# Kernel optimization log

Measured on AMD Instinct MI355X. Metric: run time of the kernel, lower is better.

The kernel has to match this reference:

```python
import jax, jax.numpy as jnp
import numpy as np

B, S, HID, H, DB = 4, 2048, 512, 8, 8
DH = HID // H  # head dim = 64


def setup_inputs() -> dict:
    key = jax.random.key(0)
    ks = jax.random.split(key, 14)
    s = 0.02
    return {
        "q": jax.random.normal(ks[0], (B, S, HID), jnp.float32),
        "k": jax.random.normal(ks[1], (B, S, HID), jnp.float32),
        "v": jax.random.normal(ks[2], (B, S, HID), jnp.float32),
        "attn_bias": jax.random.normal(ks[3], (B, S, S, DB), jnp.float32),
        "Wq": jax.random.normal(ks[4], (HID, HID), jnp.float32) * s,
        "bq": jnp.zeros((HID,), jnp.float32),
        "Wk": jax.random.normal(ks[5], (HID, HID), jnp.float32) * s,
        "bk": jnp.zeros((HID,), jnp.float32),
        "Wv": jax.random.normal(ks[6], (HID, HID), jnp.float32) * s,
        "bv": jnp.zeros((HID,), jnp.float32),
        "Wb": jax.random.normal(ks[7], (H, DB), jnp.float32) * s,
        "bb": jnp.zeros((H,), jnp.float32),
        "Wo": jax.random.normal(ks[8], (HID, HID), jnp.float32) * s,
        "bo": jnp.zeros((HID,), jnp.float32),
    }


def reference(q, k, v, attn_bias, Wq, bq, Wk, bk, Wv, bv, Wb, bb, Wo, bo):
    scale = DH ** (-0.5)
    # projections: torch Linear is x @ W.T + b
    qh = (q @ Wq.T + bq).reshape(B, S, H, DH).transpose(0, 2, 1, 3)  # [B,H,S,D]
    kh = (k @ Wk.T + bk).reshape(B, S, H, DH).transpose(0, 2, 1, 3)
    vh = (v @ Wv.T + bv).reshape(B, S, H, DH).transpose(0, 2, 1, 3)
    scores = jnp.einsum("bhqd,bhkd->bhqk", qh * scale, kh)  # [B,H,S,S]
    bias = (attn_bias @ Wb.T + bb).transpose(0, 3, 1, 2)  # [B,H,S,S]
    attn = jax.nn.softmax(scores + bias, axis=-1)
    out = jnp.einsum("bhqk,bhkd->bhqd", attn, vh)  # [B,H,S,D]
    out = out.transpose(0, 2, 1, 3).reshape(B, S, HID)
    return out @ Wo.T + bo
```

## Files before the change

kernel.cpp:

```cpp
#include <hip/hip_runtime.h>
#include <cstdint>
#include <cstddef>

#define BB 4
#define SS 2048
#define HIDD 512
#define HH 8
#define DHH 64
#define DBB 8

typedef __attribute__((ext_vector_type(4))) float f32x4;
typedef __attribute__((ext_vector_type(8))) short s16x8;
typedef __attribute__((ext_vector_type(4))) short s16x4;

__device__ __forceinline__ short f2bf(float x) {
  unsigned u = __builtin_bit_cast(unsigned, x);
  u += 0x7FFFu + ((u >> 16) & 1u);
  return (short)(u >> 16);
}
__device__ __forceinline__ float bf2f(short s) {
  unsigned u = ((unsigned)(unsigned short)s) << 16;
  return __builtin_bit_cast(float, u);
}

template <int MODE>
__global__ __launch_bounds__(256) void gemm_xwT(const float* __restrict__ X,
                                                const float* __restrict__ W,
                                                const float* __restrict__ bias,
                                                float* __restrict__ outF,
                                                short* __restrict__ outB) {
  __shared__ short xs[64][40];
  __shared__ short wsh[64][40];
  const int tid = threadIdx.x;
  const int wave = tid >> 6, lane = tid & 63;
  const int quad = lane >> 4, m16 = lane & 15;
  const int m0 = blockIdx.x * 64, n0 = blockIdx.y * 64;
  const int wm = (wave & 1) * 32, wn = (wave >> 1) * 32;

  f32x4 acc[2][2];
#pragma unroll
  for (int a = 0; a < 2; a++)
#pragma unroll
    for (int b2 = 0; b2 < 2; b2++) acc[a][b2] = (f32x4){0.f, 0.f, 0.f, 0.f};

  for (int k0 = 0; k0 < HIDD; k0 += 32) {
#pragma unroll
    for (int i = 0; i < 2; i++) {
      int c = tid + i * 256;
      int row = c >> 3, kc = c & 7;
      f32x4 xv = *(const f32x4*)(X + (size_t)(m0 + row) * HIDD + k0 + kc * 4);
      f32x4 wv = *(const f32x4*)(W + (size_t)(n0 + row) * HIDD + k0 + kc * 4);
      s16x4 xb, wb2;
#pragma unroll
      for (int j = 0; j < 4; j++) { xb[j] = f2bf(xv[j]); wb2[j] = f2bf(wv[j]); }
      *(s16x4*)(&xs[row][kc * 4]) = xb;
      *(s16x4*)(&wsh[row][kc * 4]) = wb2;
    }
    __syncthreads();
    s16x8 af[2], bfr[2];
    af[0] = *(const s16x8*)(&xs[wm + m16][quad * 8]);
    af[1] = *(const s16x8*)(&xs[wm + 16 + m16][quad * 8]);
    bfr[0] = *(const s16x8*)(&wsh[wn + m16][quad * 8]);
    bfr[1] = *(const s16x8*)(&wsh[wn + 16 + m16][quad * 8]);
    acc[0][0] = __builtin_amdgcn_mfma_f32_16x16x32_bf16(af[0], bfr[0], acc[0][0], 0, 0, 0);
    acc[0][1] = __builtin_amdgcn_mfma_f32_16x16x32_bf16(af[0], bfr[1], acc[0][1], 0, 0, 0);
    acc[1][0] = __builtin_amdgcn_mfma_f32_16x16x32_bf16(af[1], bfr[0], acc[1][0], 0, 0, 0);
    acc[1][1] = __builtin_amdgcn_mfma_f32_16x16x32_bf16(af[1], bfr[1], acc[1][1], 0, 0, 0);
    __syncthreads();
  }

#pragma unroll
  for (int a = 0; a < 2; a++)
#pragma unroll
    for (int b2 = 0; b2 < 2; b2++)
#pragma unroll
      for (int r = 0; r < 4; r++) {
        int m = m0 + wm + a * 16 + quad * 4 + r;
        int n = n0 + wn + b2 * 16 + m16;
        float val = acc[a][b2][r] + bias[n];
        if (MODE == 0) {
          int b_ = m >> 11, s = m & 2047, h = n >> 6, d = n & 63;
          outB[((size_t)(b_ * HH + h) * SS + s) * DHH + d] = f2bf(val * 0.125f);
        } else if (MODE == 1) {
          int b_ = m >> 11, s = m & 2047, h = n >> 6, d = n & 63;
          outB[((size_t)(b_ * HH + h) * SS + s) * DHH + d] = f2bf(val);
        } else if (MODE == 2) {
          int b_ = m >> 11, s = m & 2047, h = n >> 6, d = n & 63;
          outB[((size_t)(b_ * HH + h) * DHH + d) * SS + s] = f2bf(val);
        } else {
          outF[(size_t)m * HIDD + n] = val;
        }
      }
}

__global__ __launch_bounds__(512) void flash_attn(const short* __restrict__ qh,
                                                  const short* __restrict__ kh,
                                                  const short* __restrict__ vh,
                                                  const float* __restrict__ attn_bias,
                                                  const float* __restrict__ Wb,
                                                  const float* __restrict__ bb,
                                                  float* __restrict__ attn_out) {
  __shared__ short kv[20480];
  __shared__ short bp[HH][16][34];
  __shared__ short pbuf[8][16][40];
  __shared__ float wbs[72];

  const int tid = threadIdx.x;
  const int wave = tid >> 6, lane = tid & 63;
  const int quad = lane >> 4, m16 = lane & 15;
  const int b = blockIdx.x >> 7;
  const int q0 = (blockIdx.x & 127) << 4;
  const int h = wave;

  if (tid < 72) wbs[tid] = (tid < 64) ? Wb[tid] : bb[tid - 64];

  const size_t qoff = ((size_t)((b * HH + h) * SS) + q0 + m16) * DHH;
  s16x8 qf0 = *(const s16x8*)(qh + qoff + quad * 8);
  s16x8 qf1 = *(const s16x8*)(qh + qoff + 32 + quad * 8);

  f32x4 oacc[4];
#pragma unroll
  for (int dt = 0; dt < 4; dt++) oacc[dt] = (f32x4){0.f, 0.f, 0.f, 0.f};
  float m_r[4], l_r[4];
#pragma unroll
  for (int r = 0; r < 4; r++) { m_r[r] = -3.0e38f; l_r[r] = 0.f; }

  __syncthreads();

  for (int k0 = 0; k0 < SS; k0 += 32) {
#pragma unroll
    for (int i = 0; i < 4; i++) {
      int c = tid + i * 512;
      int key = c >> 6, rest = c & 63;
      int hh2 = rest >> 3, dc = rest & 7;
      s16x8 val = *(const s16x8*)(kh + ((size_t)((b * HH + hh2) * SS) + k0 + key) * DHH + dc * 8);
      *(s16x8*)(&kv[key * 520 + hh2 * 64 + dc * 8]) = val;
    }
    {
      int ql = tid >> 5, kl = tid & 31;
      const float* bptr = attn_bias + ((size_t)(b * SS + q0 + ql) * SS + k0 + kl) * DBB;
      f32x4 b0 = *(const f32x4*)(bptr);
      f32x4 b1 = *(const f32x4*)(bptr + 4);
#pragma unroll
      for (int h2 = 0; h2 < 8; h2++) {
        float a2 = wbs[64 + h2];
#pragma unroll
        for (int d = 0; d < 4; d++) {
          a2 += b0[d] * wbs[h2 * 8 + d];
          a2 += b1[d] * wbs[h2 * 8 + 4 + d];
        }
        bp[h2][ql][kl] = f2bf(a2);
      }
    }
    __syncthreads();

    f32x4 sc[2];
#pragma unroll
    for (int nt = 0; nt < 2; nt++) {
      s16x8 kf0 = *(const s16x8*)(&kv[(nt * 16 + m16) * 520 + h * 64 + quad * 8]);
      s16x8 kf1 = *(const s16x8*)(&kv[(nt * 16 + m16) * 520 + h * 64 + 32 + quad * 8]);
      f32x4 z = (f32x4){0.f, 0.f, 0.f, 0.f};
      z = __builtin_amdgcn_mfma_f32_16x16x32_bf16(qf0, kf0, z, 0, 0, 0);
      z = __builtin_amdgcn_mfma_f32_16x16x32_bf16(qf1, kf1, z, 0, 0, 0);
      sc[nt] = z;
    }

#pragma unroll
    for (int r = 0; r < 4; r++) {
      int row = quad * 4 + r;
      float s0 = sc[0][r] + bf2f(bp[h][row][m16]);
      float s1 = sc[1][r] + bf2f(bp[h][row][16 + m16]);
      float v = fmaxf(s0, s1);
      v = fmaxf(v, __shfl_xor(v, 1, 16));
      v = fmaxf(v, __shfl_xor(v, 2, 16));
      v = fmaxf(v, __shfl_xor(v, 4, 16));
      v = fmaxf(v, __shfl_xor(v, 8, 16));
      float nm = fmaxf(m_r[r], v);
      float al = __expf(m_r[r] - nm);
      m_r[r] = nm;
      float p0 = __expf(s0 - nm);
      float p1 = __expf(s1 - nm);
      float rs = p0 + p1;
      rs += __shfl_xor(rs, 1, 16);
      rs += __shfl_xor(rs, 2, 16);
      rs += __shfl_xor(rs, 4, 16);
      rs += __shfl_xor(rs, 8, 16);
      l_r[r] = l_r[r] * al + rs;
#pragma unroll
      for (int dt = 0; dt < 4; dt++) oacc[dt][r] *= al;
      pbuf[wave][row][m16] = f2bf(p0);
      pbuf[wave][row][16 + m16] = f2bf(p1);
    }
    __syncthreads();

#pragma unroll
    for (int i = 0; i < 4; i++) {
      int c = tid + i * 512;
      int d = c >> 2, kc = c & 3;
      s16x8 val = *(const s16x8*)(vh + ((size_t)((b * HH + (d >> 6)) * DHH + (d & 63)) * SS) + k0 + kc * 8);
      *(s16x8*)(&kv[d * 40 + kc * 8]) = val;
    }
    __syncthreads();

    s16x8 pf = *(const s16x8*)(&pbuf[wave][m16][quad * 8]);
#pragma unroll
    for (int dt = 0; dt < 4; dt++) {
      s16x8 vf = *(const s16x8*)(&kv[(h * 64 + dt * 16 + m16) * 40 + quad * 8]);
      oacc[dt] = __builtin_amdgcn_mfma_f32_16x16x32_bf16(pf, vf, oacc[dt], 0, 0, 0);
    }
    __syncthreads();
  }

#pragma unroll
  for (int dt = 0; dt < 4; dt++)
#pragma unroll
    for (int r = 0; r < 4; r++) {
      float val = oacc[dt][r] / l_r[r];
      attn_out[(size_t)(b * SS + q0 + quad * 4 + r) * HIDD + h * 64 + dt * 16 + m16] = val;
    }
}

extern "C" void kernel_launch(void* const* d_in, const int* in_sizes, int n_in,
                              void* d_out, int out_size, void* d_ws, size_t ws_size,
                              hipStream_t stream) {
  const float* q = (const float*)d_in[0];
  const float* k = (const float*)d_in[1];
  const float* v = (const float*)d_in[2];
  const float* attn_bias = (const float*)d_in[3];
  const float* Wq = (const float*)d_in[4];
  const float* bq = (const float*)d_in[5];
  const float* Wk = (const float*)d_in[6];
  const float* bk = (const float*)d_in[7];
  const float* Wv = (const float*)d_in[8];
  const float* bv = (const float*)d_in[9];
  const float* Wb = (const float*)d_in[10];
  const float* bb = (const float*)d_in[11];
  const float* Wo = (const float*)d_in[12];
  const float* bo = (const float*)d_in[13];
  float* out = (float*)d_out;

  short* qh = (short*)d_ws;
  short* kh = qh + (size_t)4194304;
  short* vh = kh + (size_t)4194304;
  float* attn_ws = (float*)(vh + (size_t)4194304);

  dim3 g(128, 8), blk(256);
  gemm_xwT<0><<<g, blk, 0, stream>>>(q, Wq, bq, nullptr, qh);
  gemm_xwT<1><<<g, blk, 0, stream>>>(k, Wk, bk, nullptr, kh);
  gemm_xwT<2><<<g, blk, 0, stream>>>(v, Wv, bv, nullptr, vh);
  flash_attn<<<512, 512, 0, stream>>>(qh, kh, vh, attn_bias, Wb, bb, attn_ws);
  gemm_xwT<3><<<g, blk, 0, stream>>>(attn_ws, Wo, bo, out, nullptr);
}
```

Before: 1.032 ms.

## Load K/V fragments directly from global and double-buffer bias projection

Removes the shared-memory staging of K and V tiles, so each wave reads its MFMA fragments straight from global memory. The bias projection becomes double-buffered: the next tile's attn_bias is prefetched into registers and projected after the PV MFMA, cutting four barriers per iteration down to one. Blocks are remapped to interleave batches and query tiles across XCDs, and launch bounds request higher occupancy. In exchange, K/V reuse across waves in LDS is lost, so global/L2 traffic per wave rises, and relying on the wave's own pbuf write-then-read without a barrier assumes intra-wave ordering.

```diff
diff --git a/kernel.cpp b/kernel.cpp
--- a/kernel.cpp
+++ b/kernel.cpp
@@ -93,31 +93,35 @@
       }
 }
 
-__global__ __launch_bounds__(512) void flash_attn(const short* __restrict__ qh,
-                                                  const short* __restrict__ kh,
-                                                  const short* __restrict__ vh,
-                                                  const float* __restrict__ attn_bias,
-                                                  const float* __restrict__ Wb,
-                                                  const float* __restrict__ bb,
-                                                  float* __restrict__ attn_out) {
-  __shared__ short kv[20480];
-  __shared__ short bp[HH][16][34];
-  __shared__ short pbuf[8][16][40];
-  __shared__ float wbs[72];
+__global__ __launch_bounds__(512, 8) void flash_attn(const short* __restrict__ qh,
+                                                     const short* __restrict__ kh,
+                                                     const short* __restrict__ vh,
+                                                     const float* __restrict__ attn_bias,
+                                                     const float* __restrict__ Wb,
+                                                     const float* __restrict__ bb,
+                                                     float* __restrict__ attn_out) {
+  __shared__ short bp[2][HH][16][34];
+  __shared__ short pbuf[HH][16][40];
 
   const int tid = threadIdx.x;
   const int wave = tid >> 6, lane = tid & 63;
   const int quad = lane >> 4, m16 = lane & 15;
-  const int b = blockIdx.x >> 7;
-  const int q0 = (blockIdx.x & 127) << 4;
+  const int wg = (int)blockIdx.x;
+  const int lb = ((wg & 7) << 6) | (wg >> 3);
+  const int b = lb >> 7;
+  const int q0 = (lb & 127) << 4;
   const int h = wave;
-
-  if (tid < 72) wbs[tid] = (tid < 64) ? Wb[tid] : bb[tid - 64];
 
   const size_t qoff = ((size_t)((b * HH + h) * SS) + q0 + m16) * DHH;
   s16x8 qf0 = *(const s16x8*)(qh + qoff + quad * 8);
   s16x8 qf1 = *(const s16x8*)(qh + qoff + 32 + quad * 8);
 
+  const short* kbase = kh + ((size_t)(b * HH + h) * SS + m16) * DHH + quad * 8;
+  const short* vbase = vh + ((size_t)((b * HH + h) * DHH) + m16) * SS + quad * 8;
+
+  const int ql = tid >> 5, kl = tid & 31;
+  const float* bptr = attn_bias + ((size_t)(b * SS + q0 + ql) * SS + kl) * DBB;
+
   f32x4 oacc[4];
 #pragma unroll
   for (int dt = 0; dt < 4; dt++) oacc[dt] = (f32x4){0.f, 0.f, 0.f, 0.f};
@@ -125,40 +129,39 @@
 #pragma unroll
   for (int r = 0; r < 4; r++) { m_r[r] = -3.0e38f; l_r[r] = 0.f; }
 
+  {
+    f32x4 c0 = *(const f32x4*)(bptr);
+    f32x4 c1 = *(const f32x4*)(bptr + 4);
+#pragma unroll
+    for (int h2 = 0; h2 < 8; h2++) {
+      float a2 = bb[h2];
+#pragma unroll
+      for (int d = 0; d < 4; d++) {
+        a2 += c0[d] * Wb[h2 * 8 + d];
+        a2 += c1[d] * Wb[h2 * 8 + 4 + d];
+      }
+      bp[0][h2][ql][kl] = f2bf(a2);
+    }
+  }
   __syncthreads();
 
-  for (int k0 = 0; k0 < SS; k0 += 32) {
-#pragma unroll
-    for (int i = 0; i < 4; i++) {
-      int c = tid + i * 512;
-      int key = c >> 6, rest = c & 63;
-      int hh2 = rest >> 3, dc = rest & 7;
-      s16x8 val = *(const s16x8*)(kh + ((size_t)((b * HH + hh2) * SS) + k0 + key) * DHH + dc * 8);
-      *(s16x8*)(&kv[key * 520 + hh2 * 64 + dc * 8]) = val;
-    }
-    {
-      int ql = tid >> 5, kl = tid & 31;
-      const float* bptr = attn_bias + ((size_t)(b * SS + q0 + ql) * SS + k0 + kl) * DBB;
-      f32x4 b0 = *(const f32x4*)(bptr);
-      f32x4 b1 = *(const f32x4*)(bptr + 4);
-#pragma unroll
-      for (int h2 = 0; h2 < 8; h2++) {
-        float a2 = wbs[64 + h2];
-#pragma unroll
-        for (int d = 0; d < 4; d++) {
-          a2 += b0[d] * wbs[h2 * 8 + d];
-          a2 += b1[d] * wbs[h2 * 8 + 4 + d];
-        }
-        bp[h2][ql][kl] = f2bf(a2);
-      }
-    }
-    __syncthreads();
+  for (int it = 0; it < 64; ++it) {
+    const int k0 = it << 5;
+    const int cur = it & 1;
+
+    f32x4 n0, n1;
+    if (it < 63) {
+      const float* np = bptr + (size_t)(k0 + 32) * DBB;
+      n0 = *(const f32x4*)(np);
+      n1 = *(const f32x4*)(np + 4);
+    }
 
     f32x4 sc[2];
 #pragma unroll
     for (int nt = 0; nt < 2; nt++) {
-      s16x8 kf0 = *(const s16x8*)(&kv[(nt * 16 + m16) * 520 + h * 64 + quad * 8]);
-      s16x8 kf1 = *(const s16x8*)(&kv[(nt * 16 + m16) * 520 + h * 64 + 32 + quad * 8]);
+      const short* kp = kbase + (size_t)(k0 + nt * 16) * DHH;
+      s16x8 kf0 = *(const s16x8*)(kp);
+      s16x8 kf1 = *(const s16x8*)(kp + 32);
       f32x4 z = (f32x4){0.f, 0.f, 0.f, 0.f};
       z = __builtin_amdgcn_mfma_f32_16x16x32_bf16(qf0, kf0, z, 0, 0, 0);
       z = __builtin_amdgcn_mfma_f32_16x16x32_bf16(qf1, kf1, z, 0, 0, 0);
@@ -168,8 +171,8 @@
 #pragma unroll
     for (int r = 0; r < 4; r++) {
       int row = quad * 4 + r;
-      float s0 = sc[0][r] + bf2f(bp[h][row][m16]);
-      float s1 = sc[1][r] + bf2f(bp[h][row][16 + m16]);
+      float s0 = sc[0][r] + bf2f(bp[cur][h][row][m16]);
+      float s1 = sc[1][r] + bf2f(bp[cur][h][row][16 + m16]);
       float v = fmaxf(s0, s1);
       v = fmaxf(v, __shfl_xor(v, 1, 16));
       v = fmaxf(v, __shfl_xor(v, 2, 16));
@@ -191,22 +194,26 @@
       pbuf[wave][row][m16] = f2bf(p0);
       pbuf[wave][row][16 + m16] = f2bf(p1);
     }
-    __syncthreads();
-
-#pragma unroll
-    for (int i = 0; i < 4; i++) {
-      int c = tid + i * 512;
-      int d = c >> 2, kc = c & 3;
-      s16x8 val = *(const s16x8*)(vh + ((size_t)((b * HH + (d >> 6)) * DHH + (d & 63)) * SS) + k0 + kc * 8);
-      *(s16x8*)(&kv[d * 40 + kc * 8]) = val;
-    }
-    __syncthreads();
 
     s16x8 pf = *(const s16x8*)(&pbuf[wave][m16][quad * 8]);
 #pragma unroll
     for (int dt = 0; dt < 4; dt++) {
-      s16x8 vf = *(const s16x8*)(&kv[(h * 64 + dt * 16 + m16) * 40 + quad * 8]);
+      const short* vp = vbase + (size_t)(dt * 16) * SS + k0;
+      s16x8 vf = *(const s16x8*)(vp);
       oacc[dt] = __builtin_amdgcn_mfma_f32_16x16x32_bf16(pf, vf, oacc[dt], 0, 0, 0);
+    }
+
+    if (it < 63) {
+#pragma unroll
+      for (int h2 = 0; h2 < 8; h2++) {
+        float a2 = bb[h2];
+#pragma unroll
+        for (int d = 0; d < 4; d++) {
+          a2 += n0[d] * Wb[h2 * 8 + d];
+          a2 += n1[d] * Wb[h2 * 8 + 4 + d];
+        }
+        bp[cur ^ 1][h2][ql][kl] = f2bf(a2);
+      }
     }
     __syncthreads();
   }
```

After: 1.216 ms. 17.8% more time.
